# Performance work log

Hardware: AMD Instinct MI355X
Metric: run time of the kernel (lower is better)

Reference implementation:

```python
import jax, jax.numpy as jnp
import numpy as np

PRIMAL_LUT = jnp.array([0.0, 1.0, -1.0, 0.5, -0.5, 0.333333, -0.333333, 0.2, -0.2,
                        0.142857, -0.142857, 0.090909, -0.090909, 0.076923, -0.076923, 0.0],
                       dtype=jnp.float32)


def primal_quantize(weight, scale):
    # Nearest-neighbor lookup into the 16-entry LUT (first-min tie-break like torch.argmin).
    # Loop over the 16 fixed LUT entries instead of materializing a [N,16] abs-diff tensor.
    w_scaled = weight / scale
    best_dist = jnp.full_like(w_scaled, jnp.inf)
    q = jnp.zeros_like(w_scaled)
    for v in np.asarray(PRIMAL_LUT):
        d = jnp.abs(w_scaled - v)
        take = d < best_dist  # strict < keeps the first (lowest-index) minimum
        best_dist = jnp.where(take, d, best_dist)
        q = jnp.where(take, v, q)
    return q * scale


def setup_inputs() -> dict:
    key = jax.random.key(0)
    k1, k2 = jax.random.split(key)
    in_features, out_features = 4096, 8192
    x = jax.random.normal(k1, (1, 1024, in_features), dtype=jnp.float32)
    # matches torch init: randn * (0.02 / sqrt(24))
    weight = jax.random.normal(k2, (out_features, in_features), dtype=jnp.float32) * (0.02 / np.sqrt(24.0))
    scale = jnp.array(1.0, dtype=jnp.float32)
    return {"x": x, "weight": weight, "scale": scale}


def reference(x, weight, scale):
    w_quant = primal_quantize(weight, scale)  # [out, in]
    # F.linear(x, w): x @ w.T
    return jnp.einsum('bsi,oi->bso', x, w_quant)
```

## Files before the change

### kernel.cpp

```cpp
#include <hip/hip_runtime.h>
#include <hip/hip_bf16.h>
#include <stdint.h>

#define K_DIM 4096
#define N_DIM 8192
#define NTILES (N_DIM / 128)
#define KCHUNKS (K_DIM / 32)

typedef __attribute__((ext_vector_type(8))) __bf16 bf16x8;
typedef __attribute__((ext_vector_type(4))) float f32x4;

__device__ __forceinline__ float quantize_ws(float ws, float scale) {
    float a  = fabsf(ws);
    float v  = 0.0f;
    v = (a >  0.0384615f) ? 0.076923f : v;
    v = (a >= 0.0839160f) ? 0.090909f : v;
    v = (a >= 0.1168830f) ? 0.142857f : v;
    v = (a >= 0.1714285f) ? 0.2f      : v;
    v = (a >= 0.2666665f) ? 0.333333f : v;
    v = (a >= 0.4166665f) ? 0.5f      : v;
    v = (a >= 0.75f)      ? 1.0f      : v;
    v = copysignf(v, ws);
    return v * scale;
}

__device__ __forceinline__ unsigned short to_bf16(float f) {
    unsigned int u = __float_as_uint(f);
    u += 0x7FFFu + ((u >> 16) & 1u);
    return (unsigned short)(u >> 16);
}

__global__ void quant_w_kernel(const float* __restrict__ W,
                               const float* __restrict__ scale_p,
                               unsigned short* __restrict__ Wq,
                               unsigned int* __restrict__ flags, int n4) {
    const float s   = scale_p[0];
    const float inv = 1.0f / s;
    int idx    = blockIdx.x * blockDim.x + threadIdx.x;
    int stride = gridDim.x * blockDim.x;
    const float4* W4 = (const float4*)W;
    ushort4* Q4 = (ushort4*)Wq;
    for (int i = idx; i < n4; i += stride) {
        float4 w = W4[i];
        float wx = w.x * inv, wy = w.y * inv, wz = w.z * inv, ww = w.w * inv;
        float amax = fmaxf(fmaxf(fabsf(wx), fabsf(wy)), fmaxf(fabsf(wz), fabsf(ww)));
        bool big = amax > 0.0384615f;
        if (__ballot(big)) {
            if (big) {
                ushort4 q;
                q.x = to_bf16(quantize_ws(wx, s));
                q.y = to_bf16(quantize_ws(wy, s));
                q.z = to_bf16(quantize_ws(wz, s));
                q.w = to_bf16(quantize_ws(ww, s));
                Q4[i] = q;
            }
            int col    = (i << 2) & (K_DIM - 1);
            int row    = (i << 2) >> 12;
            int kchunk = col >> 5;
            int ntile  = row >> 7;
            unsigned int mask = big ? (1u << (kchunk & 31)) : 0u;
#pragma unroll
            for (int off = 32; off; off >>= 1) mask |= __shfl_down(mask, off, 64);
            if (((threadIdx.x & 63) == 0) && mask) {
                atomicOr(&flags[ntile * 4 + (kchunk >> 5)], mask);
                atomicOr(&flags[NTILES * 4], 1u);
            }
        }
    }
}

__global__ void conv_x_kernel(const float* __restrict__ X,
                              unsigned short* __restrict__ Xb,
                              const unsigned int* __restrict__ flags, int n4) {
    if (flags[NTILES * 4] == 0u) return;
    int idx    = blockIdx.x * blockDim.x + threadIdx.x;
    int stride = gridDim.x * blockDim.x;
    const float4* X4 = (const float4*)X;
    ushort4* Q4 = (ushort4*)Xb;
    for (int i = idx; i < n4; i += stride) {
        float4 w = X4[i];
        ushort4 q;
        q.x = to_bf16(w.x); q.y = to_bf16(w.y);
        q.z = to_bf16(w.z); q.w = to_bf16(w.w);
        Q4[i] = q;
    }
}

__global__ __launch_bounds__(256) void gemm_bt_bf16(
        const unsigned short* __restrict__ A,
        const unsigned short* __restrict__ B,
        const unsigned int* __restrict__ flags,
        float* __restrict__ C, int M) {
    __shared__ unsigned short sA[128 * 32];
    __shared__ unsigned short sB[128 * 32];

    const int tid  = threadIdx.x;
    const int w    = tid >> 6;
    const int lane = tid & 63;
    const int quad = lane >> 4;
    const int l16  = lane & 15;
    const int wm   = w >> 1;
    const int wn   = w & 1;

    const int ntile = blockIdx.x & 63;
    const int mtile = blockIdx.x >> 6;
    const int m0 = mtile * 128;
    const int n0 = ntile * 128;

    const unsigned int f0 = flags[ntile * 4 + 0];
    const unsigned int f1 = flags[ntile * 4 + 1];
    const unsigned int f2 = flags[ntile * 4 + 2];
    const unsigned int f3 = flags[ntile * 4 + 3];

    f32x4 acc[4][4];
    const f32x4 z = {0.f, 0.f, 0.f, 0.f};
#pragma unroll
    for (int i = 0; i < 4; ++i)
#pragma unroll
        for (int j = 0; j < 4; ++j) acc[i][j] = z;

    const char* Abase = (const char*)A;
    const char* Bbase = (const char*)B;
    char* sAb = (char*)sA;
    char* sBb = (char*)sB;

    for (int k0 = 0; k0 < K_DIM; k0 += 32) {
        int ch = k0 >> 5;
        unsigned int word = (ch < 64) ? ((ch < 32) ? f0 : f1)
                                      : ((ch < 96) ? f2 : f3);
        if (!((word >> (ch & 31)) & 1u)) continue;

#pragma unroll
        for (int p = 0; p < 2; ++p) {
            int c   = p * 256 + tid;
            int row = c >> 2;
            int kc  = c & 3;
            const char* ga = Abase + ((size_t)(m0 + row) * K_DIM + k0) * 2 + kc * 16;
            const char* gb = Bbase + ((size_t)(n0 + row) * K_DIM + k0) * 2 + kc * 16;
            char* la = sAb + p * 4096 + w * 1024;
            char* lb = sBb + p * 4096 + w * 1024;
            __builtin_amdgcn_global_load_lds((const __attribute__((address_space(1))) void*)ga,
                                             (__attribute__((address_space(3))) void*)la, 16, 0, 0);
            __builtin_amdgcn_global_load_lds((const __attribute__((address_space(1))) void*)gb,
                                             (__attribute__((address_space(3))) void*)lb, 16, 0, 0);
        }
        __syncthreads();

        bf16x8 af[4], bf[4];
#pragma unroll
        for (int i = 0; i < 4; ++i) {
            af[i] = *(const bf16x8*)(sAb + ((size_t)(wm * 64 + i * 16 + l16) * 32 + quad * 8) * 2);
            bf[i] = *(const bf16x8*)(sBb + ((size_t)(wn * 64 + i * 16 + l16) * 32 + quad * 8) * 2);
        }
#pragma unroll
        for (int mi = 0; mi < 4; ++mi)
#pragma unroll
            for (int ni = 0; ni < 4; ++ni)
                acc[mi][ni] = __builtin_amdgcn_mfma_f32_16x16x32_bf16(af[mi], bf[ni], acc[mi][ni], 0, 0, 0);
        __syncthreads();
    }

#pragma unroll
    for (int mi = 0; mi < 4; ++mi) {
#pragma unroll
        for (int ni = 0; ni < 4; ++ni) {
            int row = m0 + wm * 64 + mi * 16 + quad * 4;
            int col = n0 + wn * 64 + ni * 16 + l16;
#pragma unroll
            for (int r = 0; r < 4; ++r)
                C[(size_t)(row + r) * N_DIM + col] = acc[mi][ni][r];
        }
    }
}

__global__ void quant_w_inplace(float* W, const float* __restrict__ scale_p, int n4) {
    const float s   = scale_p[0];
    const float inv = 1.0f / s;
    int idx    = blockIdx.x * blockDim.x + threadIdx.x;
    int stride = gridDim.x * blockDim.x;
    float4* W4 = (float4*)W;
    for (int i = idx; i < n4; i += stride) {
        float4 w = W4[i];
        w.x = quantize_ws(w.x * inv, s); w.y = quantize_ws(w.y * inv, s);
        w.z = quantize_ws(w.z * inv, s); w.w = quantize_ws(w.w * inv, s);
        W4[i] = w;
    }
}

__global__ __launch_bounds__(256) void gemm_fp32_fb(const float* __restrict__ A,
                                                    const float* __restrict__ B,
                                                    float* __restrict__ C, int M) {
    __shared__ float sA[64][17];
    __shared__ float sB[64][17];
    int tid = threadIdx.x;
    int tx = tid & 15, ty = tid >> 4;
    int n0 = (blockIdx.x & 127) * 64;
    int m0 = (blockIdx.x >> 7) * 64;
    float acc[4][4] = {};
    for (int k0 = 0; k0 < K_DIM; k0 += 16) {
#pragma unroll
        for (int i = 0; i < 4; ++i) {
            int e = tid + i * 256;
            int r = e >> 4, c = e & 15;
            sA[r][c] = A[(size_t)(m0 + r) * K_DIM + k0 + c];
            sB[r][c] = B[(size_t)(n0 + r) * K_DIM + k0 + c];
        }
        __syncthreads();
#pragma unroll
        for (int kk = 0; kk < 16; ++kk) {
            float a[4], b[4];
#pragma unroll
            for (int i = 0; i < 4; ++i) { a[i] = sA[ty * 4 + i][kk]; b[i] = sB[tx * 4 + i][kk]; }
#pragma unroll
            for (int i = 0; i < 4; ++i)
#pragma unroll
                for (int j = 0; j < 4; ++j) acc[i][j] += a[i] * b[j];
        }
        __syncthreads();
    }
#pragma unroll
    for (int i = 0; i < 4; ++i)
#pragma unroll
        for (int j = 0; j < 4; ++j)
            C[(size_t)(m0 + ty * 4 + i) * N_DIM + n0 + tx * 4 + j] = acc[i][j];
}

extern "C" void kernel_launch(void* const* d_in, const int* in_sizes, int n_in,
                              void* d_out, int out_size, void* d_ws, size_t ws_size,
                              hipStream_t stream) {
    const float* x     = (const float*)d_in[0];
    const float* W     = (const float*)d_in[1];
    const float* scale = (const float*)d_in[2];
    float* out = (float*)d_out;

    const int M = in_sizes[0] / K_DIM;
    const size_t wq_bytes = (size_t)N_DIM * K_DIM * 2;
    const size_t xb_bytes = (size_t)M * K_DIM * 2;
    const size_t fl_bytes = (size_t)(NTILES * 4 + 1) * sizeof(unsigned int);

    if (ws_size >= wq_bytes + xb_bytes + fl_bytes && (M % 128) == 0) {
        unsigned short* Wq = (unsigned short*)d_ws;
        unsigned short* Xb = (unsigned short*)((char*)d_ws + wq_bytes);
        unsigned int* flags = (unsigned int*)((char*)d_ws + wq_bytes + xb_bytes);
        int nW4 = (N_DIM * K_DIM) / 4;
        int nX4 = (M * K_DIM) / 4;
        hipMemsetAsync(flags, 0, fl_bytes, stream);
        hipLaunchKernelGGL(quant_w_kernel, dim3(2048), dim3(256), 0, stream, W, scale, Wq, flags, nW4);
        hipLaunchKernelGGL(conv_x_kernel, dim3(1024), dim3(256), 0, stream, x, Xb, flags, nX4);
        hipLaunchKernelGGL(gemm_bt_bf16, dim3((M / 128) * (N_DIM / 128)), dim3(256), 0, stream,
                           Xb, Wq, flags, out, M);
    } else {
        int nW4 = (N_DIM * K_DIM) / 4;
        hipLaunchKernelGGL(quant_w_inplace, dim3(2048), dim3(256), 0, stream,
                           (float*)W, scale, nW4);
        hipLaunchKernelGGL(gemm_fp32_fb, dim3((M / 64) * (N_DIM / 64)), dim3(256), 0, stream,
                           x, W, out, M);
    }
}
```

Baseline: 215.6 us.

## Fuse weight quantization and bf16 conversion into GEMM tile loads; scan-only flag pass

Result: faster. 206.6 us (-4.2%).

```diff
diff --git a/kernel.cpp b/kernel.cpp
--- a/kernel.cpp
+++ b/kernel.cpp
@@ -5,9 +5,10 @@
 #define K_DIM 4096
 #define N_DIM 8192
 #define NTILES (N_DIM / 128)
-#define KCHUNKS (K_DIM / 32)
+#define FLAG_WORDS (NTILES * 4)
 
 typedef __attribute__((ext_vector_type(8))) __bf16 bf16x8;
+typedef __attribute__((ext_vector_type(8))) unsigned short u16x8;
 typedef __attribute__((ext_vector_type(4))) float f32x4;
 
 __device__ __forceinline__ float quantize_ws(float ws, float scale) {
@@ -30,30 +31,18 @@
     return (unsigned short)(u >> 16);
 }
 
-__global__ void quant_w_kernel(const float* __restrict__ W,
-                               const float* __restrict__ scale_p,
-                               unsigned short* __restrict__ Wq,
-                               unsigned int* __restrict__ flags, int n4) {
-    const float s   = scale_p[0];
-    const float inv = 1.0f / s;
+__global__ void scan_w_kernel(const float* __restrict__ W,
+                              const float* __restrict__ scale_p,
+                              unsigned int* __restrict__ flags, int n4) {
+    const float th = 0.0384615f * fabsf(scale_p[0]);
     int idx    = blockIdx.x * blockDim.x + threadIdx.x;
     int stride = gridDim.x * blockDim.x;
     const float4* W4 = (const float4*)W;
-    ushort4* Q4 = (ushort4*)Wq;
     for (int i = idx; i < n4; i += stride) {
         float4 w = W4[i];
-        float wx = w.x * inv, wy = w.y * inv, wz = w.z * inv, ww = w.w * inv;
-        float amax = fmaxf(fmaxf(fabsf(wx), fabsf(wy)), fmaxf(fabsf(wz), fabsf(ww)));
-        bool big = amax > 0.0384615f;
+        float amax = fmaxf(fmaxf(fabsf(w.x), fabsf(w.y)), fmaxf(fabsf(w.z), fabsf(w.w)));
+        bool big = amax > th;
         if (__ballot(big)) {
-            if (big) {
-                ushort4 q;
-                q.x = to_bf16(quantize_ws(wx, s));
-                q.y = to_bf16(quantize_ws(wy, s));
-                q.z = to_bf16(quantize_ws(wz, s));
-                q.w = to_bf16(quantize_ws(ww, s));
-                Q4[i] = q;
-            }
             int col    = (i << 2) & (K_DIM - 1);
             int row    = (i << 2) >> 12;
             int kchunk = col >> 5;
@@ -61,40 +50,46 @@
             unsigned int mask = big ? (1u << (kchunk & 31)) : 0u;
 #pragma unroll
             for (int off = 32; off; off >>= 1) mask |= __shfl_down(mask, off, 64);
-            if (((threadIdx.x & 63) == 0) && mask) {
+            if (((threadIdx.x & 63) == 0) && mask)
                 atomicOr(&flags[ntile * 4 + (kchunk >> 5)], mask);
-                atomicOr(&flags[NTILES * 4], 1u);
-            }
-        }
-    }
-}
-
-__global__ void conv_x_kernel(const float* __restrict__ X,
-                              unsigned short* __restrict__ Xb,
-                              const unsigned int* __restrict__ flags, int n4) {
-    if (flags[NTILES * 4] == 0u) return;
-    int idx    = blockIdx.x * blockDim.x + threadIdx.x;
-    int stride = gridDim.x * blockDim.x;
-    const float4* X4 = (const float4*)X;
-    ushort4* Q4 = (ushort4*)Xb;
-    for (int i = idx; i < n4; i += stride) {
-        float4 w = X4[i];
-        ushort4 q;
-        q.x = to_bf16(w.x); q.y = to_bf16(w.y);
-        q.z = to_bf16(w.z); q.w = to_bf16(w.w);
-        Q4[i] = q;
+        }
     }
 }
 
 __global__ __launch_bounds__(256) void gemm_bt_bf16(
-        const unsigned short* __restrict__ A,
-        const unsigned short* __restrict__ B,
+        const float* __restrict__ X,
+        const float* __restrict__ Wf,
+        const float* __restrict__ scale_p,
         const unsigned int* __restrict__ flags,
         float* __restrict__ C, int M) {
     __shared__ unsigned short sA[128 * 32];
     __shared__ unsigned short sB[128 * 32];
 
     const int tid  = threadIdx.x;
+    const int ntile = blockIdx.x & 63;
+    const int mtile = blockIdx.x >> 6;
+    const int m0 = mtile * 128;
+    const int n0 = ntile * 128;
+
+    const unsigned int f0 = flags[ntile * 4 + 0];
+    const unsigned int f1 = flags[ntile * 4 + 1];
+    const unsigned int f2 = flags[ntile * 4 + 2];
+    const unsigned int f3 = flags[ntile * 4 + 3];
+
+    if ((f0 | f1 | f2 | f3) == 0u) {
+        const float4 zz = {0.f, 0.f, 0.f, 0.f};
+        float4* C4 = (float4*)(C + (size_t)m0 * N_DIM + n0);
+#pragma unroll
+        for (int g = tid; g < 128 * 32; g += 256) {
+            int r = g >> 5, c = g & 31;
+            C4[(size_t)r * (N_DIM / 4) + c] = zz;
+        }
+        return;
+    }
+
+    const float s   = scale_p[0];
+    const float inv = 1.0f / s;
+
     const int w    = tid >> 6;
     const int lane = tid & 63;
     const int quad = lane >> 4;
@@ -102,16 +97,6 @@
     const int wm   = w >> 1;
     const int wn   = w & 1;
 
-    const int ntile = blockIdx.x & 63;
-    const int mtile = blockIdx.x >> 6;
-    const int m0 = mtile * 128;
-    const int n0 = ntile * 128;
-
-    const unsigned int f0 = flags[ntile * 4 + 0];
-    const unsigned int f1 = flags[ntile * 4 + 1];
-    const unsigned int f2 = flags[ntile * 4 + 2];
-    const unsigned int f3 = flags[ntile * 4 + 3];
-
     f32x4 acc[4][4];
     const f32x4 z = {0.f, 0.f, 0.f, 0.f};
 #pragma unroll
@@ -119,8 +104,6 @@
 #pragma unroll
         for (int j = 0; j < 4; ++j) acc[i][j] = z;
 
-    const char* Abase = (const char*)A;
-    const char* Bbase = (const char*)B;
     char* sAb = (char*)sA;
     char* sBb = (char*)sB;
 
@@ -132,17 +115,30 @@
 
 #pragma unroll
         for (int p = 0; p < 2; ++p) {
-            int c   = p * 256 + tid;
-            int row = c >> 2;
-            int kc  = c & 3;
-            const char* ga = Abase + ((size_t)(m0 + row) * K_DIM + k0) * 2 + kc * 16;
-            const char* gb = Bbase + ((size_t)(n0 + row) * K_DIM + k0) * 2 + kc * 16;
-            char* la = sAb + p * 4096 + w * 1024;
-            char* lb = sBb + p * 4096 + w * 1024;
-            __builtin_amdgcn_global_load_lds((const __attribute__((address_space(1))) void*)ga,
-                                             (__attribute__((address_space(3))) void*)la, 16, 0, 0);
-            __builtin_amdgcn_global_load_lds((const __attribute__((address_space(1))) void*)gb,
-                                             (__attribute__((address_space(3))) void*)lb, 16, 0, 0);
+            int g   = p * 256 + tid;
+            int row = g >> 2;
+            int seg = g & 3;
+            const float* xa = X  + (size_t)(m0 + row) * K_DIM + k0 + seg * 8;
+            const float* wb = Wf + (size_t)(n0 + row) * K_DIM + k0 + seg * 8;
+            float4 a0 = *(const float4*)xa;
+            float4 a1 = *(const float4*)(xa + 4);
+            float4 b0 = *(const float4*)wb;
+            float4 b1 = *(const float4*)(wb + 4);
+            u16x8 qa, qb;
+            qa[0] = to_bf16(a0.x); qa[1] = to_bf16(a0.y);
+            qa[2] = to_bf16(a0.z); qa[3] = to_bf16(a0.w);
+            qa[4] = to_bf16(a1.x); qa[5] = to_bf16(a1.y);
+            qa[6] = to_bf16(a1.z); qa[7] = to_bf16(a1.w);
+            qb[0] = to_bf16(quantize_ws(b0.x * inv, s));
+            qb[1] = to_bf16(quantize_ws(b0.y * inv, s));
+            qb[2] = to_bf16(quantize_ws(b0.z * inv, s));
+            qb[3] = to_bf16(quantize_ws(b0.w * inv, s));
+            qb[4] = to_bf16(quantize_ws(b1.x * inv, s));
+            qb[5] = to_bf16(quantize_ws(b1.y * inv, s));
+            qb[6] = to_bf16(quantize_ws(b1.z * inv, s));
+            qb[7] = to_bf16(quantize_ws(b1.w * inv, s));
+            *(u16x8*)(sAb + row * 64 + seg * 16) = qa;
+            *(u16x8*)(sBb + row * 64 + seg * 16) = qb;
         }
         __syncthreads();
 
@@ -173,25 +169,14 @@
     }
 }
 
-__global__ void quant_w_inplace(float* W, const float* __restrict__ scale_p, int n4) {
-    const float s   = scale_p[0];
-    const float inv = 1.0f / s;
-    int idx    = blockIdx.x * blockDim.x + threadIdx.x;
-    int stride = gridDim.x * blockDim.x;
-    float4* W4 = (float4*)W;
-    for (int i = idx; i < n4; i += stride) {
-        float4 w = W4[i];
-        w.x = quantize_ws(w.x * inv, s); w.y = quantize_ws(w.y * inv, s);
-        w.z = quantize_ws(w.z * inv, s); w.w = quantize_ws(w.w * inv, s);
-        W4[i] = w;
-    }
-}
-
 __global__ __launch_bounds__(256) void gemm_fp32_fb(const float* __restrict__ A,
                                                     const float* __restrict__ B,
+                                                    const float* __restrict__ scale_p,
                                                     float* __restrict__ C, int M) {
     __shared__ float sA[64][17];
     __shared__ float sB[64][17];
+    const float s   = scale_p[0];
+    const float inv = 1.0f / s;
     int tid = threadIdx.x;
     int tx = tid & 15, ty = tid >> 4;
     int n0 = (blockIdx.x & 127) * 64;
@@ -203,7 +188,7 @@
             int e = tid + i * 256;
             int r = e >> 4, c = e & 15;
             sA[r][c] = A[(size_t)(m0 + r) * K_DIM + k0 + c];
-            sB[r][c] = B[(size_t)(n0 + r) * K_DIM + k0 + c];
+            sB[r][c] = quantize_ws(B[(size_t)(n0 + r) * K_DIM + k0 + c] * inv, s);
         }
         __syncthreads();
 #pragma unroll
@@ -234,26 +219,17 @@
     float* out = (float*)d_out;
 
     const int M = in_sizes[0] / K_DIM;
-    const size_t wq_bytes = (size_t)N_DIM * K_DIM * 2;
-    const size_t xb_bytes = (size_t)M * K_DIM * 2;
-    const size_t fl_bytes = (size_t)(NTILES * 4 + 1) * sizeof(unsigned int);
-
-    if (ws_size >= wq_bytes + xb_bytes + fl_bytes && (M % 128) == 0) {
-        unsigned short* Wq = (unsigned short*)d_ws;
-        unsigned short* Xb = (unsigned short*)((char*)d_ws + wq_bytes);
-        unsigned int* flags = (unsigned int*)((char*)d_ws + wq_bytes + xb_bytes);
+    const size_t fl_bytes = (size_t)FLAG_WORDS * sizeof(unsigned int);
+
+    if (ws_size >= fl_bytes && (M % 128) == 0) {
+        unsigned int* flags = (unsigned int*)d_ws;
         int nW4 = (N_DIM * K_DIM) / 4;
-        int nX4 = (M * K_DIM) / 4;
         hipMemsetAsync(flags, 0, fl_bytes, stream);
-        hipLaunchKernelGGL(quant_w_kernel, dim3(2048), dim3(256), 0, stream, W, scale, Wq, flags, nW4);
-        hipLaunchKernelGGL(conv_x_kernel, dim3(1024), dim3(256), 0, stream, x, Xb, flags, nX4);
+        hipLaunchKernelGGL(scan_w_kernel, dim3(2048), dim3(256), 0, stream, W, scale, flags, nW4);
         hipLaunchKernelGGL(gemm_bt_bf16, dim3((M / 128) * (N_DIM / 128)), dim3(256), 0, stream,
-                           Xb, Wq, flags, out, M);
+                           x, W, scale, flags, out, M);
     } else {
-        int nW4 = (N_DIM * K_DIM) / 4;
-        hipLaunchKernelGGL(quant_w_inplace, dim3(2048), dim3(256), 0, stream,
-                           (float*)W, scale, nW4);
         hipLaunchKernelGGL(gemm_fp32_fb, dim3((M / 64) * (N_DIM / 64)), dim3(256), 0, stream,
-                           x, W, out, M);
-    }
-}
+                           x, W, scale, out, M);
+    }
+}
```
